# Kernel optimization log

Measured on AMD Instinct MI355X. Metric: run time of the kernel, lower is better.

## Reference

```python
import jax, jax.numpy as jnp
import numpy as np

N, E, De, Dv = 40000, 8000, 32, 8   # nodes, hyperedges, edge degree, node degree
D, Q, EIG, VOC, NC = 256, 256, 64, 1000, 40  # vertex/edge dim, query dim, eig dim, centrality vocab, classes
LN_EPS = 1e-5


def _linear(x, W, b):
    return x @ W + b


def _layernorm(x, g, b):
    mu = jnp.mean(x, axis=-1, keepdims=True)
    var = jnp.mean(jnp.square(x - mu), axis=-1, keepdims=True)
    return (x - mu) * jax.lax.rsqrt(var + LN_EPS) * g + b


def setup_inputs() -> dict:
    key = jax.random.key(0)
    ks = iter(jax.random.split(key, 64))
    def nrm(shape, s=0.02):
        return (jax.random.normal(next(ks), shape, jnp.float32) * s).astype(jnp.float32)
    inp = {
        'vfeat': jax.random.normal(next(ks), (N, D), jnp.float32),
        'efeat': jax.random.normal(next(ks), (E, D), jnp.float32),
        'eign_vec': jax.random.normal(next(ks), (N, EIG), jnp.float32),
        'feat_v_gcn': jax.random.normal(next(ks), (N, D), jnp.float32),
        'cent1': jax.random.uniform(next(ks), (E, De), jnp.float32),
        'cent2': jax.random.uniform(next(ks), (N, Dv), jnp.float32),
        'cent_idx': jax.random.randint(next(ks), (N,), 0, VOC),
        'uniq_idx': jax.random.randint(next(ks), (N,), 0, VOC),
        'edge2node': jax.random.randint(next(ks), (E, De), 0, N),
        'node2edge': jax.random.randint(next(ks), (N, Dv), 0, E),
        # learned parameters (W: [in, out])
        'W_vtx': nrm((D, D)), 'b_vtx': jnp.zeros((D,), jnp.float32),
        'W_pe': nrm((EIG, D)), 'b_pe': jnp.zeros((D,), jnp.float32),
        'cs_emb': nrm((VOC, D)), 'un_emb': nrm((VOC, D)),
        'W_kv': nrm((D, Q)), 'b_kv': jnp.zeros((Q,), jnp.float32),
        'W_vv': nrm((D, D)), 'b_vv': jnp.zeros((D,), jnp.float32),
        'W_qe': nrm((D, Q)), 'b_qe': jnp.zeros((Q,), jnp.float32),
        'W_ke': nrm((D, Q)), 'b_ke': jnp.zeros((Q,), jnp.float32),
        'W_ve': nrm((D, D)), 'b_ve': jnp.zeros((D,), jnp.float32),
        'W_qv': nrm((D, Q)), 'b_qv': jnp.zeros((Q,), jnp.float32),
        'W_l1': nrm((D, Q)), 'b_l1': jnp.zeros((Q,), jnp.float32),
        'W_l2': nrm((Q, D)), 'b_l2': jnp.zeros((D,), jnp.float32),
        'W_l3': nrm((D, Q)), 'b_l3': jnp.zeros((Q,), jnp.float32),
        'W_l4': nrm((Q, D)), 'b_l4': jnp.zeros((D,), jnp.float32),
        'ln1_g': jnp.ones((D,), jnp.float32), 'ln1_b': jnp.zeros((D,), jnp.float32),
        'ln2_g': jnp.ones((D,), jnp.float32), 'ln2_b': jnp.zeros((D,), jnp.float32),
        'W_cls': nrm((D, NC)), 'b_cls': jnp.zeros((NC,), jnp.float32),
    }
    return inp


def _forward(vfeat, efeat, eign_vec, feat_v_gcn, cent1, cent2,
             W_vtx, b_vtx, W_pe, b_pe, cs_emb, un_emb,
             W_kv, b_kv, W_vv, b_vv, W_qe, b_qe, W_ke, b_ke, W_ve, b_ve, W_qv, b_qv,
             W_l1, b_l1, W_l2, b_l2, W_l3, b_l3, W_l4, b_l4,
             ln1_g, ln1_b, ln2_g, ln2_b, W_cls, b_cls,
             cent_idx, uniq_idx, edge2node, node2edge):
    scale = 1.0 / np.sqrt(float(W_kv.shape[1]))  # 1/sqrt(query_dim)
    # first_layer feature assembly: vtx_lin_1layer + PE + GCN + centrality/uniqueness embeddings
    feat_v = (_linear(vfeat, W_vtx, b_vtx) + _linear(eign_vec, W_pe, b_pe)
              + feat_v_gcn + cs_emb[cent_idx] + un_emb[uniq_idx])
    feat_e = efeat

    # ---- stage 1: hyperedges attend over member nodes ('in' etype) ----
    k_n = _linear(feat_v, W_kv, b_kv)              # [N,Q]
    v_n = _linear(feat_v, W_vv, b_vv)              # [N,D]
    q_e = _linear(feat_e, W_qe, b_qe)              # [E,Q]
    km = k_n[edge2node]                            # [E,De,Q]
    attn = jax.nn.leaky_relu(jnp.einsum('edq,eq->ed', km, q_e), 0.01) * scale
    score = jax.nn.softmax(attn + cent1, axis=1)   # centrality-biased softmax (k-core + clustering)
    h_e = jnp.einsum('ed,edc->ec', score, v_n[edge2node])  # [E,D]
    x_e = _layernorm(h_e + feat_e, ln1_g, ln1_b)
    f_e = _linear(jax.nn.relu(_linear(x_e, W_l1, b_l1)), W_l2, b_l2)
    feat_e = _layernorm(f_e + x_e, ln1_g, ln1_b)

    # ---- stage 2: nodes attend over incident hyperedges ('con' etype) ----
    k_e = _linear(feat_e, W_ke, b_ke)              # [E,Q]
    v_e = _linear(feat_e, W_ve, b_ve)              # [E,D]
    q_v = _linear(feat_v, W_qv, b_qv)              # [N,Q]
    km2 = k_e[node2edge]                           # [N,Dv,Q]
    attn2 = jax.nn.leaky_relu(jnp.einsum('ndq,nq->nd', km2, q_v), 0.01) * scale
    score2 = jax.nn.softmax(attn2 + cent2, axis=1)
    h_v = jnp.einsum('nd,ndc->nc', score2, v_e[node2edge])  # [N,D]
    x_v = _layernorm(h_v + feat_v, ln2_g, ln2_b)
    f_v = _linear(jax.nn.relu(_linear(x_v, W_l3, b_l3)), W_l4, b_l4)
    feat_v = _layernorm(f_v + x_v, ln2_g, ln2_b)

    # last_layer classification head (dropout is identity in eval)
    return _linear(feat_v, W_cls, b_cls)           # [N,NC]


def reference(vfeat, efeat, eign_vec, feat_v_gcn, cent1, cent2,
              cent_idx, uniq_idx, edge2node, node2edge,
              W_vtx, b_vtx, W_pe, b_pe, cs_emb, un_emb,
              W_kv, b_kv, W_vv, b_vv, W_qe, b_qe, W_ke, b_ke, W_ve, b_ve, W_qv, b_qv,
              W_l1, b_l1, W_l2, b_l2, W_l3, b_l3, W_l4, b_l4,
              ln1_g, ln1_b, ln2_g, ln2_b, W_cls, b_cls):
    return _forward(vfeat, efeat, eign_vec, feat_v_gcn, cent1, cent2,
                    W_vtx, b_vtx, W_pe, b_pe, cs_emb, un_emb,
                    W_kv, b_kv, W_vv, b_vv, W_qe, b_qe, W_ke, b_ke, W_ve, b_ve, W_qv, b_qv,
                    W_l1, b_l1, W_l2, b_l2, W_l3, b_l3, W_l4, b_l4,
                    ln1_g, ln1_b, ln2_g, ln2_b, W_cls, b_cls,
                    cent_idx, uniq_idx, edge2node, node2edge)
```

## Files before the change

kernel.cpp:

```cpp
#include <hip/hip_runtime.h>
#include <hip/hip_bf16.h>
#include <cstddef>

#define N_NODES 40000
#define N_EDGES 8000
#define DE 32
#define DV 8
#define DIM 256
#define QDIM 256
#define EIGD 64
#define NCLS 40
#define LN_EPS 1e-5f
#define ATT_SCALE 0.0625f

typedef unsigned short u16;
typedef unsigned int u32;
using i16x8 = __attribute__((ext_vector_type(8))) short;
using f32x4 = __attribute__((ext_vector_type(4))) float;

__device__ inline u16 f2b(float f) {
    union { float f; u32 u; } c; c.f = f;
    u32 u = c.u + 0x7FFF + ((c.u >> 16) & 1);
    return (u16)(u >> 16);
}
__device__ inline float b2f(u16 b) {
    union { u32 u; float f; } c; c.u = (u32)b << 16;
    return c.f;
}

__device__ inline void gload_lds16(const u16* g, u16* l) {
    __builtin_amdgcn_global_load_lds(
        (const __attribute__((address_space(1))) void*)g,
        (__attribute__((address_space(3))) void*)l, 16, 0, 0);
}

#define VMCNT6 asm volatile("s_waitcnt vmcnt(6)" ::: "memory")
#define VMCNT0 asm volatile("s_waitcnt vmcnt(0)" ::: "memory")
#define LGKM0  asm volatile("s_waitcnt lgkmcnt(0)" ::: "memory")

__global__ __launch_bounds__(256) void cast_bf16(
    const float* __restrict__ src, u16* __restrict__ dst, int n4)
{
    for (int i = blockIdx.x * 256 + threadIdx.x; i < n4; i += gridDim.x * 256) {
        float4 v = ((const float4*)src)[i];
        ushort4 o;
        o.x = f2b(v.x); o.y = f2b(v.y); o.z = f2b(v.z); o.w = f2b(v.w);
        ((ushort4*)dst)[i] = o;
    }
}

__global__ __launch_bounds__(256) void prep_weights(
    const float* w0, const float* w1, const float* w2, const float* w3,
    const float* w4, const float* w5, const float* w6, const float* w7,
    const float* w8, const float* w9, const float* w10, const float* w11,
    const float* w12, u16* __restrict__ pool)
{
    const float* srcs[13] = {w0,w1,w2,w3,w4,w5,w6,w7,w8,w9,w10,w11,w12};
    const int Ks[13]  = {256,64,256,256,256,256,256,256,256,256,256,256,256};
    const int Nds[13] = {256,256,256,256,256,256,256,256,256,256,256,256,40};
    const int id = blockIdx.z;
    const float* W = srcs[id];
    u16* Wt = pool + (size_t)id * 65536;
    const int K = Ks[id], Nd = Nds[id];
    const int k0 = blockIdx.x * 32, n0 = blockIdx.y * 32;
    if (k0 >= K || n0 >= Nd) return;

    __shared__ float tile[32][33];
    const int x = threadIdx.x & 31, y4 = (threadIdx.x >> 5) * 4;
#pragma unroll
    for (int j = 0; j < 4; j++) {
        int k = k0 + y4 + j;
        tile[y4 + j][x] = (k < K && (n0 + x) < Nd) ? W[(size_t)k * Nd + n0 + x] : 0.f;
    }
    __syncthreads();
#pragma unroll
    for (int j = 0; j < 4; j++) {
        int n = n0 + y4 + j;
        if (n < Nd && (k0 + x) < K)
            Wt[(size_t)n * K + k0 + x] = f2b(tile[x][y4 + j]);
    }
}

template <int EPI>
__global__ __launch_bounds__(256) void gemm_mfma(
    const u16* __restrict__ A, const u16* __restrict__ Wt,
    const float* __restrict__ bias, const float* __restrict__ bias2,
    const u16* __restrict__ resid,
    const float* __restrict__ gcn, const float* __restrict__ emb1,
    const float* __restrict__ emb2, const int* __restrict__ idx1,
    const int* __restrict__ idx2,
    void* __restrict__ Cv, int M, int K, int Nd)
{
    __shared__ u16 Asm[2][64 * 64];
    __shared__ u16 Bsm[2][128 * 64];
    const int t = threadIdx.x;
    const int lane = t & 63, w = t >> 6;
    const int wr = w >> 1, wc = w & 1;
    const int row0 = blockIdx.y * 64, col0 = blockIdx.x * 128;

    f32x4 acc[2][4] = {};

    const int srow = lane >> 3;
    const int sblk = ((lane & 7) ^ srow) * 8;

    const int fr = lane & 15, h = lane >> 4;
    const int lsw = fr & 7;
    const int nt = K >> 6;

    auto stage = [&](int buf, int kt) {
        const int k0 = kt << 6;
#pragma unroll
        for (int i = 0; i < 2; i++) {
            int r = w * 16 + i * 8;
            const u16* gp = A + (size_t)(row0 + r + srow) * K + k0 + sblk;
            gload_lds16(gp, &Asm[buf][r * 64]);
        }
#pragma unroll
        for (int i = 0; i < 4; i++) {
            int r = w * 32 + i * 8;
            int ng = col0 + r + srow; if (ng > Nd - 1) ng = Nd - 1;
            const u16* gp = Wt + (size_t)ng * K + k0 + sblk;
            gload_lds16(gp, &Bsm[buf][r * 64]);
        }
    };

    stage(0, 0);
    for (int kt = 0; kt < nt; ++kt) {
        const int cur = kt & 1;
        const bool more = (kt + 1 < nt);
        if (more) stage(cur ^ 1, kt + 1);
        if (more) { VMCNT6; } else { VMCNT0; }
        __builtin_amdgcn_s_barrier();

        i16x8 af[2][2], bf[2][4];
#pragma unroll
        for (int kk = 0; kk < 2; kk++) {
#pragma unroll
            for (int m = 0; m < 2; m++)
                af[kk][m] = *(const i16x8*)&Asm[cur][(wr * 32 + m * 16 + fr) * 64 +
                                                    ((kk * 4 + h) ^ lsw) * 8];
#pragma unroll
            for (int n = 0; n < 4; n++)
                bf[kk][n] = *(const i16x8*)&Bsm[cur][(wc * 64 + n * 16 + fr) * 64 +
                                                    ((kk * 4 + h) ^ lsw) * 8];
        }
        LGKM0;
        __builtin_amdgcn_sched_barrier(0);
        __builtin_amdgcn_s_barrier();

#pragma unroll
        for (int kk = 0; kk < 2; kk++)
#pragma unroll
            for (int m = 0; m < 2; m++)
#pragma unroll
                for (int n = 0; n < 4; n++)
                    acc[m][n] = __builtin_amdgcn_mfma_f32_16x16x32_bf16(
                        af[kk][m], bf[kk][n], acc[m][n], 0, 0, 0);
    }

#pragma unroll
    for (int m = 0; m < 2; m++) {
#pragma unroll
        for (int j = 0; j < 4; j++) {
            const int grow = row0 + wr * 32 + m * 16 + h * 4 + j;
            int i1 = 0, i2 = 0;
            if constexpr (EPI == 3) { i1 = idx1[grow]; i2 = idx2[grow]; }
#pragma unroll
            for (int n = 0; n < 4; n++) {
                const int gcol = col0 + wc * 64 + n * 16 + fr;
                if (EPI == 4 && gcol >= Nd) continue;
                float v = acc[m][n][j] +
                          (gcol < 256 ? bias[gcol] : bias2[gcol - 256]);
                if constexpr (EPI == 1) v = fmaxf(v, 0.f);
                if constexpr (EPI == 2)
                    v += b2f(resid[(size_t)grow * Nd + gcol]);
                if constexpr (EPI == 3) {
                    v += b2f(resid[(size_t)grow * Nd + gcol]);
                    v += gcn[(size_t)grow * Nd + gcol];
                    v += emb1[(size_t)i1 * Nd + gcol];
                    v += emb2[(size_t)i2 * Nd + gcol];
                }
                if constexpr (EPI == 4)
                    ((float*)Cv)[(size_t)grow * Nd + gcol] = v;
                else
                    ((u16*)Cv)[(size_t)grow * Nd + gcol] = f2b(v);
            }
        }
    }
}

__device__ inline float bfly_sum(float v) {
#pragma unroll
    for (int off = 32; off; off >>= 1) v += __shfl_xor(v, off, 64);
    return v;
}

__global__ __launch_bounds__(256) void edge_attn(
    const u16* __restrict__ KVn, const u16* __restrict__ QE,
    const float* __restrict__ efeat,
    const int* __restrict__ e2n, const float* __restrict__ cent1,
    const float* __restrict__ g, const float* __restrict__ bb,
    u16* __restrict__ XE)
{
    const int lane = threadIdx.x & 63, w = threadIdx.x >> 6;
    const int e = blockIdx.x * 4 + w;
    const int c4 = lane * 4;

    ushort4 q4 = *(const ushort4*)&QE[(size_t)e * QDIM + c4];
    const float q0 = b2f(q4.x), q1 = b2f(q4.y), q2 = b2f(q4.z), q3 = b2f(q4.w);

    int rows[DE]; float sc[DE];
#pragma unroll
    for (int d = 0; d < DE; d++) rows[d] = e2n[(size_t)e * DE + d];
#pragma unroll
    for (int d = 0; d < DE; d++) {
        ushort4 k4 = *(const ushort4*)&KVn[(size_t)rows[d] * 512 + c4];
        float p = q0 * b2f(k4.x) + q1 * b2f(k4.y) + q2 * b2f(k4.z) + q3 * b2f(k4.w);
        p = bfly_sum(p);
        sc[d] = (p > 0.f ? p : 0.01f * p) * ATT_SCALE + cent1[(size_t)e * DE + d];
    }
    float mx = sc[0];
#pragma unroll
    for (int d = 1; d < DE; d++) mx = fmaxf(mx, sc[d]);
    float s = 0.f;
#pragma unroll
    for (int d = 0; d < DE; d++) { sc[d] = __expf(sc[d] - mx); s += sc[d]; }
    const float inv = 1.f / s;

    float a0 = 0.f, a1 = 0.f, a2 = 0.f, a3 = 0.f;
#pragma unroll
    for (int d = 0; d < DE; d++) {
        ushort4 v4 = *(const ushort4*)&KVn[(size_t)rows[d] * 512 + 256 + c4];
        float sd = sc[d] * inv;
        a0 = fmaf(sd, b2f(v4.x), a0); a1 = fmaf(sd, b2f(v4.y), a1);
        a2 = fmaf(sd, b2f(v4.z), a2); a3 = fmaf(sd, b2f(v4.w), a3);
    }
    float4 ef = *(const float4*)&efeat[(size_t)e * DIM + c4];
    float x0 = a0 + ef.x, x1 = a1 + ef.y, x2 = a2 + ef.z, x3 = a3 + ef.w;

    float mu = bfly_sum(x0 + x1 + x2 + x3) * (1.f / DIM);
    float d0 = x0 - mu, d1 = x1 - mu, d2 = x2 - mu, d3 = x3 - mu;
    float var = bfly_sum(d0 * d0 + d1 * d1 + d2 * d2 + d3 * d3) * (1.f / DIM);
    float r = rsqrtf(var + LN_EPS);
    float4 gv = *(const float4*)&g[c4];
    float4 bv = *(const float4*)&bb[c4];
    ushort4 o;
    o.x = f2b(d0 * r * gv.x + bv.x); o.y = f2b(d1 * r * gv.y + bv.y);
    o.z = f2b(d2 * r * gv.z + bv.z); o.w = f2b(d3 * r * gv.w + bv.w);
    *(ushort4*)&XE[(size_t)e * DIM + c4] = o;
}

__global__ __launch_bounds__(256) void node_attn(
    const u16* __restrict__ KVe, const u16* __restrict__ QV,
    const u16* __restrict__ FV,
    const int* __restrict__ n2e, const float* __restrict__ cent2,
    const float* __restrict__ g, const float* __restrict__ bb,
    u16* __restrict__ XV)
{
    const int lane = threadIdx.x & 63, w = threadIdx.x >> 6;
    const int n = blockIdx.x * 4 + w;
    const int c4 = lane * 4;

    ushort4 q4 = *(const ushort4*)&QV[(size_t)n * QDIM + c4];
    const float q0 = b2f(q4.x), q1 = b2f(q4.y), q2 = b2f(q4.z), q3 = b2f(q4.w);

    int rows[DV]; float sc[DV];
#pragma unroll
    for (int d = 0; d < DV; d++) rows[d] = n2e[(size_t)n * DV + d];
#pragma unroll
    for (int d = 0; d < DV; d++) {
        ushort4 k4 = *(const ushort4*)&KVe[(size_t)rows[d] * 512 + c4];
        float p = q0 * b2f(k4.x) + q1 * b2f(k4.y) + q2 * b2f(k4.z) + q3 * b2f(k4.w);
        p = bfly_sum(p);
        sc[d] = (p > 0.f ? p : 0.01f * p) * ATT_SCALE + cent2[(size_t)n * DV + d];
    }
    float mx = sc[0];
#pragma unroll
    for (int d = 1; d < DV; d++) mx = fmaxf(mx, sc[d]);
    float s = 0.f;
#pragma unroll
    for (int d = 0; d < DV; d++) { sc[d] = __expf(sc[d] - mx); s += sc[d]; }
    const float inv = 1.f / s;

    float a0 = 0.f, a1 = 0.f, a2 = 0.f, a3 = 0.f;
#pragma unroll
    for (int d = 0; d < DV; d++) {
        ushort4 v4 = *(const ushort4*)&KVe[(size_t)rows[d] * 512 + 256 + c4];
        float sd = sc[d] * inv;
        a0 = fmaf(sd, b2f(v4.x), a0); a1 = fmaf(sd, b2f(v4.y), a1);
        a2 = fmaf(sd, b2f(v4.z), a2); a3 = fmaf(sd, b2f(v4.w), a3);
    }
    ushort4 f4 = *(const ushort4*)&FV[(size_t)n * DIM + c4];
    float x0 = a0 + b2f(f4.x), x1 = a1 + b2f(f4.y);
    float x2 = a2 + b2f(f4.z), x3 = a3 + b2f(f4.w);

    float mu = bfly_sum(x0 + x1 + x2 + x3) * (1.f / DIM);
    float d0 = x0 - mu, d1 = x1 - mu, d2 = x2 - mu, d3 = x3 - mu;
    float var = bfly_sum(d0 * d0 + d1 * d1 + d2 * d2 + d3 * d3) * (1.f / DIM);
    float r = rsqrtf(var + LN_EPS);
    float4 gv = *(const float4*)&g[c4];
    float4 bv = *(const float4*)&bb[c4];
    ushort4 o;
    o.x = f2b(d0 * r * gv.x + bv.x); o.y = f2b(d1 * r * gv.y + bv.y);
    o.z = f2b(d2 * r * gv.z + bv.z); o.w = f2b(d3 * r * gv.w + bv.w);
    *(ushort4*)&XV[(size_t)n * DIM + c4] = o;
}

__global__ __launch_bounds__(256) void ln_rows(
    const u16* __restrict__ X, const float* __restrict__ g,
    const float* __restrict__ bb, u16* __restrict__ Y)
{
    const int lane = threadIdx.x & 63, w = threadIdx.x >> 6;
    const int row = blockIdx.x * 4 + w;
    const int c4 = lane * 4;
    ushort4 v4 = *(const ushort4*)&X[(size_t)row * DIM + c4];
    float x0 = b2f(v4.x), x1 = b2f(v4.y), x2 = b2f(v4.z), x3 = b2f(v4.w);
    float mu = bfly_sum(x0 + x1 + x2 + x3) * (1.f / DIM);
    float d0 = x0 - mu, d1 = x1 - mu, d2 = x2 - mu, d3 = x3 - mu;
    float var = bfly_sum(d0 * d0 + d1 * d1 + d2 * d2 + d3 * d3) * (1.f / DIM);
    float r = rsqrtf(var + LN_EPS);
    float4 gv = *(const float4*)&g[c4];
    float4 bv = *(const float4*)&bb[c4];
    ushort4 o;
    o.x = f2b(d0 * r * gv.x + bv.x); o.y = f2b(d1 * r * gv.y + bv.y);
    o.z = f2b(d2 * r * gv.z + bv.z); o.w = f2b(d3 * r * gv.w + bv.w);
    *(ushort4*)&Y[(size_t)row * DIM + c4] = o;
}

extern "C" void kernel_launch(void* const* d_in, const int* in_sizes, int n_in,
                              void* d_out, int out_size, void* d_ws, size_t ws_size,
                              hipStream_t stream)
{
    const float* vfeat  = (const float*)d_in[0];
    const float* efeat  = (const float*)d_in[1];
    const float* eign   = (const float*)d_in[2];
    const float* gcn    = (const float*)d_in[3];
    const float* cent1  = (const float*)d_in[4];
    const float* cent2  = (const float*)d_in[5];
    const int*   cidx   = (const int*)d_in[6];
    const int*   uidx   = (const int*)d_in[7];
    const int*   e2n    = (const int*)d_in[8];
    const int*   n2e    = (const int*)d_in[9];
    const float* W_vtx  = (const float*)d_in[10]; const float* b_vtx = (const float*)d_in[11];
    const float* W_pe   = (const float*)d_in[12]; const float* b_pe  = (const float*)d_in[13];
    const float* cs_emb = (const float*)d_in[14]; const float* un_emb= (const float*)d_in[15];
    const float* W_kv   = (const float*)d_in[16]; const float* b_kv  = (const float*)d_in[17];
    const float* W_vv   = (const float*)d_in[18]; const float* b_vv  = (const float*)d_in[19];
    const float* W_qe   = (const float*)d_in[20]; const float* b_qe  = (const float*)d_in[21];
    const float* W_ke   = (const float*)d_in[22]; const float* b_ke  = (const float*)d_in[23];
    const float* W_ve   = (const float*)d_in[24]; const float* b_ve  = (const float*)d_in[25];
    const float* W_qv   = (const float*)d_in[26]; const float* b_qv  = (const float*)d_in[27];
    const float* W_l1   = (const float*)d_in[28]; const float* b_l1  = (const float*)d_in[29];
    const float* W_l2   = (const float*)d_in[30]; const float* b_l2  = (const float*)d_in[31];
    const float* W_l3   = (const float*)d_in[32]; const float* b_l3  = (const float*)d_in[33];
    const float* W_l4   = (const float*)d_in[34]; const float* b_l4  = (const float*)d_in[35];
    const float* ln1_g  = (const float*)d_in[36]; const float* ln1_b = (const float*)d_in[37];
    const float* ln2_g  = (const float*)d_in[38]; const float* ln2_b = (const float*)d_in[39];
    const float* W_cls  = (const float*)d_in[40]; const float* b_cls = (const float*)d_in[41];
    float* out = (float*)d_out;

    const size_t NE = (size_t)N_NODES * DIM;
    const size_t EE = (size_t)N_EDGES * DIM;
    u16* ws = (u16*)d_ws;
    u16* FV  = ws;
    u16* T0  = FV + NE;
    u16* B2  = T0 + NE;
    u16* KVn = B2 + NE;
    u16* Vb  = KVn + 2 * NE;
    u16* Gb  = Vb + NE;
    u16* Eb  = Gb + (size_t)N_NODES * EIGD;
    u16* QEb = Eb + EE;
    u16* XE  = QEb + EE;
    u16* TE  = XE + EE;
    u16* FE  = TE + EE;
    u16* KVe = FE + EE;
    u16* Wp  = KVe + 2 * EE;
    u16* Wt_vtx = Wp +  0*65536; u16* Wt_pe = Wp +  1*65536;
    u16* Wt_kv  = Wp +  2*65536;
    u16* Wt_qe  = Wp +  4*65536; u16* Wt_ke = Wp +  5*65536;
         u16* Wt_qv = Wp +  7*65536;
    u16* Wt_l1  = Wp +  8*65536; u16* Wt_l2 = Wp +  9*65536;
    u16* Wt_l3  = Wp + 10*65536; u16* Wt_l4 = Wp + 11*65536;
    u16* Wt_cls = Wp + 12*65536;

    const dim3 blk(256);
    const dim3 gW(8, 8, 13);
    const dim3 gN1(2, N_NODES / 64);
    const dim3 gN2(4, N_NODES / 64);
    const dim3 gE1(2, N_EDGES / 64);
    const dim3 gE2(4, N_EDGES / 64);
    const dim3 gCl(1, N_NODES / 64);

    prep_weights<<<gW, blk, 0, stream>>>(
        W_vtx, W_pe, W_kv, W_vv, W_qe, W_ke, W_ve, W_qv,
        W_l1, W_l2, W_l3, W_l4, W_cls, Wp);
    cast_bf16<<<2048, blk, 0, stream>>>(vfeat, Vb, (int)(NE / 4));
    cast_bf16<<<1024, blk, 0, stream>>>(eign, Gb, N_NODES * EIGD / 4);
    cast_bf16<<<1024, blk, 0, stream>>>(efeat, Eb, (int)(EE / 4));

    gemm_mfma<0><<<gN1, blk, 0, stream>>>(Vb, Wt_vtx, b_vtx, b_vtx, nullptr,
        nullptr, nullptr, nullptr, nullptr, nullptr, T0, N_NODES, DIM, DIM);
    gemm_mfma<3><<<gN1, blk, 0, stream>>>(Gb, Wt_pe, b_pe, b_pe, T0,
        gcn, cs_emb, un_emb, cidx, uidx, FV, N_NODES, EIGD, DIM);

    gemm_mfma<0><<<gN2, blk, 0, stream>>>(FV, Wt_kv, b_kv, b_vv, nullptr,
        nullptr, nullptr, nullptr, nullptr, nullptr, KVn, N_NODES, DIM, 512);
    gemm_mfma<0><<<gE1, blk, 0, stream>>>(Eb, Wt_qe, b_qe, b_qe, nullptr,
        nullptr, nullptr, nullptr, nullptr, nullptr, QEb, N_EDGES, DIM, QDIM);
    edge_attn<<<N_EDGES / 4, blk, 0, stream>>>(KVn, QEb, efeat, e2n, cent1,
        ln1_g, ln1_b, XE);
    gemm_mfma<1><<<gE1, blk, 0, stream>>>(XE, Wt_l1, b_l1, b_l1, nullptr,
        nullptr, nullptr, nullptr, nullptr, nullptr, TE, N_EDGES, DIM, QDIM);
    gemm_mfma<2><<<gE1, blk, 0, stream>>>(TE, Wt_l2, b_l2, b_l2, XE,
        nullptr, nullptr, nullptr, nullptr, nullptr, FE, N_EDGES, QDIM, DIM);
    ln_rows<<<N_EDGES / 4, blk, 0, stream>>>(FE, ln1_g, ln1_b, FE);

    gemm_mfma<0><<<gE2, blk, 0, stream>>>(FE, Wt_ke, b_ke, b_ve, nullptr,
        nullptr, nullptr, nullptr, nullptr, nullptr, KVe, N_EDGES, DIM, 512);
    gemm_mfma<0><<<gN1, blk, 0, stream>>>(FV, Wt_qv, b_qv, b_qv, nullptr,
        nullptr, nullptr, nullptr, nullptr, nullptr, T0, N_NODES, DIM, QDIM);
    node_attn<<<N_NODES / 4, blk, 0, stream>>>(KVe, T0, FV, n2e, cent2,
        ln2_g, ln2_b, B2);
    gemm_mfma<1><<<gN1, blk, 0, stream>>>(B2, Wt_l3, b_l3, b_l3, nullptr,
        nullptr, nullptr, nullptr, nullptr, nullptr, T0, N_NODES, DIM, QDIM);
    gemm_mfma<2><<<gN1, blk, 0, stream>>>(T0, Wt_l4, b_l4, b_l4, B2,
        nullptr, nullptr, nullptr, nullptr, nullptr, FV, N_NODES, QDIM, DIM);
    ln_rows<<<N_NODES / 4, blk, 0, stream>>>(FV, ln2_g, ln2_b, FV);

    gemm_mfma<4><<<gCl, blk, 0, stream>>>(FV, Wt_cls, b_cls, b_cls, nullptr,
        nullptr, nullptr, nullptr, nullptr, nullptr, out, N_NODES, DIM, NCLS);
}
```

Baseline: 269.3 us.

## Fuse GEMMs with layernorm, merge projections, and use online softmax in attention

Measured after the change: 264.3 us. About the same (-1.9%).

```diff
diff --git a/kernel.cpp b/kernel.cpp
--- a/kernel.cpp
+++ b/kernel.cpp
@@ -34,18 +34,29 @@
         (__attribute__((address_space(3))) void*)l, 16, 0, 0);
 }
 
-#define VMCNT6 asm volatile("s_waitcnt vmcnt(6)" ::: "memory")
-#define VMCNT0 asm volatile("s_waitcnt vmcnt(0)" ::: "memory")
-#define LGKM0  asm volatile("s_waitcnt lgkmcnt(0)" ::: "memory")
-
-__global__ __launch_bounds__(256) void cast_bf16(
-    const float* __restrict__ src, u16* __restrict__ dst, int n4)
-{
-    for (int i = blockIdx.x * 256 + threadIdx.x; i < n4; i += gridDim.x * 256) {
-        float4 v = ((const float4*)src)[i];
+#define VMCNT10 asm volatile("s_waitcnt vmcnt(10)" ::: "memory")
+#define VMCNT6  asm volatile("s_waitcnt vmcnt(6)" ::: "memory")
+#define VMCNT0  asm volatile("s_waitcnt vmcnt(0)" ::: "memory")
+#define LGKM0   asm volatile("s_waitcnt lgkmcnt(0)" ::: "memory")
+
+__global__ __launch_bounds__(256) void cast_all(
+    const float* __restrict__ vfeat, const float* __restrict__ eign,
+    const float* __restrict__ efeat,
+    u16* __restrict__ Vb, u16* __restrict__ Gb, u16* __restrict__ Eb)
+{
+    const int A4 = N_NODES * DIM / 4;
+    const int B4 = N_NODES * EIGD / 4;
+    const int C4 = N_EDGES * DIM / 4;
+    const int tot = A4 + B4 + C4;
+    for (int i = blockIdx.x * 256 + threadIdx.x; i < tot; i += gridDim.x * 256) {
+        const float4* s; ushort4* d; int j;
+        if (i < A4)            { s = (const float4*)vfeat; d = (ushort4*)Vb; j = i; }
+        else if (i < A4 + B4)  { s = (const float4*)eign;  d = (ushort4*)Gb; j = i - A4; }
+        else                   { s = (const float4*)efeat; d = (ushort4*)Eb; j = i - A4 - B4; }
+        float4 v = s[j];
         ushort4 o;
         o.x = f2b(v.x); o.y = f2b(v.y); o.z = f2b(v.z); o.w = f2b(v.w);
-        ((ushort4*)dst)[i] = o;
+        d[j] = o;
     }
 }
 
@@ -81,15 +92,16 @@
     }
 }
 
-template <int EPI>
+template <int EPI, bool DUAL>
 __global__ __launch_bounds__(256) void gemm_mfma(
-    const u16* __restrict__ A, const u16* __restrict__ Wt,
-    const float* __restrict__ bias, const float* __restrict__ bias2,
-    const u16* __restrict__ resid,
+    const u16* __restrict__ A, const u16* __restrict__ A2,
+    const u16* __restrict__ Wt, const u16* __restrict__ Wt2,
+    const float* __restrict__ bias0, const float* __restrict__ bias1,
+    const float* __restrict__ bias2,
     const float* __restrict__ gcn, const float* __restrict__ emb1,
     const float* __restrict__ emb2, const int* __restrict__ idx1,
     const int* __restrict__ idx2,
-    void* __restrict__ Cv, int M, int K, int Nd)
+    void* __restrict__ Cv, int M, int K1, int Ktot, int Nd)
 {
     __shared__ u16 Asm[2][64 * 64];
     __shared__ u16 Bsm[2][128 * 64];
@@ -105,21 +117,26 @@
 
     const int fr = lane & 15, h = lane >> 4;
     const int lsw = fr & 7;
-    const int nt = K >> 6;
+    const int nt = Ktot >> 6;
 
     auto stage = [&](int buf, int kt) {
         const int k0 = kt << 6;
+        const bool first = !DUAL || (k0 < K1);
 #pragma unroll
         for (int i = 0; i < 2; i++) {
             int r = w * 16 + i * 8;
-            const u16* gp = A + (size_t)(row0 + r + srow) * K + k0 + sblk;
+            const u16* gp = first
+                ? A  + (size_t)(row0 + r + srow) * K1 + k0 + sblk
+                : A2 + (size_t)(row0 + r + srow) * 64 + (k0 - K1) + sblk;
             gload_lds16(gp, &Asm[buf][r * 64]);
         }
 #pragma unroll
         for (int i = 0; i < 4; i++) {
             int r = w * 32 + i * 8;
             int ng = col0 + r + srow; if (ng > Nd - 1) ng = Nd - 1;
-            const u16* gp = Wt + (size_t)ng * K + k0 + sblk;
+            const u16* gp = first
+                ? Wt  + (size_t)ng * K1 + k0 + sblk
+                : Wt2 + (size_t)ng * 64 + (k0 - K1) + sblk;
             gload_lds16(gp, &Bsm[buf][r * 64]);
         }
     };
@@ -169,17 +186,18 @@
             for (int n = 0; n < 4; n++) {
                 const int gcol = col0 + wc * 64 + n * 16 + fr;
                 if (EPI == 4 && gcol >= Nd) continue;
-                float v = acc[m][n][j] +
-                          (gcol < 256 ? bias[gcol] : bias2[gcol - 256]);
-                if constexpr (EPI == 1) v = fmaxf(v, 0.f);
-                if constexpr (EPI == 2)
-                    v += b2f(resid[(size_t)grow * Nd + gcol]);
+                float v;
                 if constexpr (EPI == 3) {
-                    v += b2f(resid[(size_t)grow * Nd + gcol]);
+                    v = acc[m][n][j] + bias0[gcol] + bias1[gcol];
                     v += gcn[(size_t)grow * Nd + gcol];
                     v += emb1[(size_t)i1 * Nd + gcol];
                     v += emb2[(size_t)i2 * Nd + gcol];
+                } else {
+                    const float* bp = (gcol < 256) ? bias0
+                                     : ((gcol < 512) ? bias1 : bias2);
+                    v = acc[m][n][j] + bp[gcol & 255];
                 }
+                if constexpr (EPI == 1) v = fmaxf(v, 0.f);
                 if constexpr (EPI == 4)
                     ((float*)Cv)[(size_t)grow * Nd + gcol] = v;
                 else
@@ -189,14 +207,126 @@
     }
 }
 
-__device__ inline float bfly_sum(float v) {
-#pragma unroll
-    for (int off = 32; off; off >>= 1) v += __shfl_xor(v, off, 64);
-    return v;
+__global__ __launch_bounds__(256) void gemm_ln(
+    const u16* __restrict__ A, const u16* __restrict__ Wt,
+    const float* __restrict__ bias, const u16* __restrict__ resid,
+    const float* __restrict__ g, const float* __restrict__ bb,
+    u16* __restrict__ Y, int M)
+{
+    __shared__ u16 Asm[2][64 * 64];
+    __shared__ u16 Bsm[2][256 * 64];
+    const int t = threadIdx.x;
+    const int lane = t & 63, w = t >> 6;
+    const int row0 = blockIdx.y * 64;
+
+    f32x4 acc[4][4] = {};
+
+    const int srow = lane >> 3;
+    const int sblk = ((lane & 7) ^ srow) * 8;
+    const int fr = lane & 15, h = lane >> 4;
+    const int lsw = fr & 7;
+
+    auto stage = [&](int buf, int kt) {
+        const int k0 = kt << 6;
+#pragma unroll
+        for (int i = 0; i < 2; i++) {
+            int r = w * 16 + i * 8;
+            gload_lds16(A + (size_t)(row0 + r + srow) * 256 + k0 + sblk,
+                        &Asm[buf][r * 64]);
+        }
+#pragma unroll
+        for (int i = 0; i < 8; i++) {
+            int r = w * 64 + i * 8;
+            gload_lds16(Wt + (size_t)(r + srow) * 256 + k0 + sblk,
+                        &Bsm[buf][r * 64]);
+        }
+    };
+
+    stage(0, 0);
+    for (int kt = 0; kt < 4; ++kt) {
+        const int cur = kt & 1;
+        const bool more = (kt < 3);
+        if (more) stage(cur ^ 1, kt + 1);
+        if (more) { VMCNT10; } else { VMCNT0; }
+        __builtin_amdgcn_s_barrier();
+
+        i16x8 af[2][4], bf[2][4];
+#pragma unroll
+        for (int kk = 0; kk < 2; kk++) {
+#pragma unroll
+            for (int m = 0; m < 4; m++)
+                af[kk][m] = *(const i16x8*)&Asm[cur][(m * 16 + fr) * 64 +
+                                                    ((kk * 4 + h) ^ lsw) * 8];
+#pragma unroll
+            for (int n = 0; n < 4; n++)
+                bf[kk][n] = *(const i16x8*)&Bsm[cur][(w * 64 + n * 16 + fr) * 64 +
+                                                    ((kk * 4 + h) ^ lsw) * 8];
+        }
+        LGKM0;
+        __builtin_amdgcn_sched_barrier(0);
+        __builtin_amdgcn_s_barrier();
+
+#pragma unroll
+        for (int kk = 0; kk < 2; kk++)
+#pragma unroll
+            for (int m = 0; m < 4; m++)
+#pragma unroll
+                for (int n = 0; n < 4; n++)
+                    acc[m][n] = __builtin_amdgcn_mfma_f32_16x16x32_bf16(
+                        af[kk][m], bf[kk][n], acc[m][n], 0, 0, 0);
+    }
+
+    float* redS = (float*)&Asm[0][0];
+    float* redQ = redS + 256;
+#pragma unroll
+    for (int m = 0; m < 4; m++) {
+#pragma unroll
+        for (int j = 0; j < 4; j++) {
+            const int grow = row0 + m * 16 + h * 4 + j;
+            float s = 0.f, q = 0.f;
+#pragma unroll
+            for (int n = 0; n < 4; n++) {
+                const int gcol = w * 64 + n * 16 + fr;
+                float v = acc[m][n][j] + bias[gcol] +
+                          b2f(resid[(size_t)grow * 256 + gcol]);
+                acc[m][n][j] = v;
+                s += v; q += v * v;
+            }
+#pragma unroll
+            for (int off = 1; off < 16; off <<= 1) {
+                s += __shfl_xor(s, off, 64);
+                q += __shfl_xor(q, off, 64);
+            }
+            if (fr == 0) {
+                redS[(m * 16 + h * 4 + j) * 4 + w] = s;
+                redQ[(m * 16 + h * 4 + j) * 4 + w] = q;
+            }
+        }
+    }
+    __syncthreads();
+#pragma unroll
+    for (int m = 0; m < 4; m++) {
+#pragma unroll
+        for (int j = 0; j < 4; j++) {
+            const int r = m * 16 + h * 4 + j;
+            const int grow = row0 + r;
+            float4 s4 = *(const float4*)&redS[r * 4];
+            float4 q4 = *(const float4*)&redQ[r * 4];
+            float mu = (s4.x + s4.y + s4.z + s4.w) * (1.f / DIM);
+            float var = (q4.x + q4.y + q4.z + q4.w) * (1.f / DIM) - mu * mu;
+            float rr = rsqrtf(var + LN_EPS);
+#pragma unroll
+            for (int n = 0; n < 4; n++) {
+                const int gcol = w * 64 + n * 16 + fr;
+                float y = (acc[m][n][j] - mu) * rr * g[gcol] + bb[gcol];
+                Y[(size_t)grow * 256 + gcol] = f2b(y);
+            }
+        }
+    }
 }
 
 __global__ __launch_bounds__(256) void edge_attn(
-    const u16* __restrict__ KVn, const u16* __restrict__ QE,
+    const u16* __restrict__ KVQn, const u16* __restrict__ QE,
     const float* __restrict__ efeat,
     const int* __restrict__ e2n, const float* __restrict__ cent1,
     const float* __restrict__ g, const float* __restrict__ bb,
@@ -209,49 +339,73 @@
     ushort4 q4 = *(const ushort4*)&QE[(size_t)e * QDIM + c4];
     const float q0 = b2f(q4.x), q1 = b2f(q4.y), q2 = b2f(q4.z), q3 = b2f(q4.w);
 
-    int rows[DE]; float sc[DE];
+    int rows[DE];
 #pragma unroll
     for (int d = 0; d < DE; d++) rows[d] = e2n[(size_t)e * DE + d];
-#pragma unroll
-    for (int d = 0; d < DE; d++) {
-        ushort4 k4 = *(const ushort4*)&KVn[(size_t)rows[d] * 512 + c4];
-        float p = q0 * b2f(k4.x) + q1 * b2f(k4.y) + q2 * b2f(k4.z) + q3 * b2f(k4.w);
-        p = bfly_sum(p);
-        sc[d] = (p > 0.f ? p : 0.01f * p) * ATT_SCALE + cent1[(size_t)e * DE + d];
-    }
-    float mx = sc[0];
-#pragma unroll
-    for (int d = 1; d < DE; d++) mx = fmaxf(mx, sc[d]);
-    float s = 0.f;
-#pragma unroll
-    for (int d = 0; d < DE; d++) { sc[d] = __expf(sc[d] - mx); s += sc[d]; }
-    const float inv = 1.f / s;
-
+
+    float m = -1e30f, l = 0.f;
     float a0 = 0.f, a1 = 0.f, a2 = 0.f, a3 = 0.f;
 #pragma unroll
-    for (int d = 0; d < DE; d++) {
-        ushort4 v4 = *(const ushort4*)&KVn[(size_t)rows[d] * 512 + 256 + c4];
-        float sd = sc[d] * inv;
-        a0 = fmaf(sd, b2f(v4.x), a0); a1 = fmaf(sd, b2f(v4.y), a1);
-        a2 = fmaf(sd, b2f(v4.z), a2); a3 = fmaf(sd, b2f(v4.w), a3);
-    }
+    for (int d0 = 0; d0 < DE; d0 += 4) {
+        ushort4 k4[4], v4[4]; float p[4];
+#pragma unroll
+        for (int j = 0; j < 4; j++) {
+            const u16* base = KVQn + (size_t)rows[d0 + j] * 768 + c4;
+            k4[j] = *(const ushort4*)base;
+            v4[j] = *(const ushort4*)(base + 256);
+        }
+#pragma unroll
+        for (int j = 0; j < 4; j++)
+            p[j] = q0 * b2f(k4[j].x) + q1 * b2f(k4[j].y)
+                 + q2 * b2f(k4[j].z) + q3 * b2f(k4[j].w);
+#pragma unroll
+        for (int off = 32; off; off >>= 1)
+#pragma unroll
+            for (int j = 0; j < 4; j++) p[j] += __shfl_xor(p[j], off, 64);
+#pragma unroll
+        for (int j = 0; j < 4; j++) {
+            float s = p[j];
+            s = (s > 0.f ? s : 0.01f * s) * ATT_SCALE + cent1[(size_t)e * DE + d0 + j];
+            float wgt;
+            if (s > m) {
+                float f = __expf(m - s);
+                a0 *= f; a1 *= f; a2 *= f; a3 *= f; l *= f;
+                m = s; wgt = 1.f;
+            } else {
+                wgt = __expf(s - m);
+            }
+            l += wgt;
+            a0 = fmaf(wgt, b2f(v4[j].x), a0);
+            a1 = fmaf(wgt, b2f(v4[j].y), a1);
+            a2 = fmaf(wgt, b2f(v4[j].z), a2);
+            a3 = fmaf(wgt, b2f(v4[j].w), a3);
+        }
+    }
+    const float inv = 1.f / l;
     float4 ef = *(const float4*)&efeat[(size_t)e * DIM + c4];
-    float x0 = a0 + ef.x, x1 = a1 + ef.y, x2 = a2 + ef.z, x3 = a3 + ef.w;
-
-    float mu = bfly_sum(x0 + x1 + x2 + x3) * (1.f / DIM);
-    float d0 = x0 - mu, d1 = x1 - mu, d2 = x2 - mu, d3 = x3 - mu;
-    float var = bfly_sum(d0 * d0 + d1 * d1 + d2 * d2 + d3 * d3) * (1.f / DIM);
+    float x0 = a0 * inv + ef.x, x1 = a1 * inv + ef.y;
+    float x2 = a2 * inv + ef.z, x3 = a3 * inv + ef.w;
+
+    float mu = x0 + x1 + x2 + x3;
+#pragma unroll
+    for (int off = 32; off; off >>= 1) mu += __shfl_xor(mu, off, 64);
+    mu *= (1.f / DIM);
+    float d0_ = x0 - mu, d1 = x1 - mu, d2 = x2 - mu, d3 = x3 - mu;
+    float var = d0_ * d0_ + d1 * d1 + d2 * d2 + d3 * d3;
+#pragma unroll
+    for (int off = 32; off; off >>= 1) var += __shfl_xor(var, off, 64);
+    var *= (1.f / DIM);
     float r = rsqrtf(var + LN_EPS);
     float4 gv = *(const float4*)&g[c4];
     float4 bv = *(const float4*)&bb[c4];
     ushort4 o;
-    o.x = f2b(d0 * r * gv.x + bv.x); o.y = f2b(d1 * r * gv.y + bv.y);
+    o.x = f2b(d0_ * r * gv.x + bv.x); o.y = f2b(d1 * r * gv.y + bv.y);
     o.z = f2b(d2 * r * gv.z + bv.z); o.w = f2b(d3 * r * gv.w + bv.w);
     *(ushort4*)&XE[(size_t)e * DIM + c4] = o;
 }
 
 __global__ __launch_bounds__(256) void node_attn(
-    const u16* __restrict__ KVe, const u16* __restrict__ QV,
+    const u16* __restrict__ KVe, const u16* __restrict__ KVQn,
     const u16* __restrict__ FV,
     const int* __restrict__ n2e, const float* __restrict__ cent2,
     const float* __restrict__ g, const float* __restrict__ bb,
@@ -261,42 +415,62 @@
     const int n = blockIdx.x * 4 + w;
     const int c4 = lane * 4;
 
-    ushort4 q4 = *(const ushort4*)&QV[(size_t)n * QDIM + c4];
+    ushort4 q4 = *(const ushort4*)&KVQn[(size_t)n * 768 + 512 + c4];
     const float q0 = b2f(q4.x), q1 = b2f(q4.y), q2 = b2f(q4.z), q3 = b2f(q4.w);
 
-    int rows[DV]; float sc[DV];
+    int rows[DV];
 #pragma unroll
     for (int d = 0; d < DV; d++) rows[d] = n2e[(size_t)n * DV + d];
+
+    ushort4 k4[DV], v4[DV];
 #pragma unroll
     for (int d = 0; d < DV; d++) {
-        ushort4 k4 = *(const ushort4*)&KVe[(size_t)rows[d] * 512 + c4];
-        float p = q0 * b2f(k4.x) + q1 * b2f(k4.y) + q2 * b2f(k4.z) + q3 * b2f(k4.w);
-        p = bfly_sum(p);
-        sc[d] = (p > 0.f ? p : 0.01f * p) * ATT_SCALE + cent2[(size_t)n * DV + d];
-    }
-    float mx = sc[0];
-#pragma unroll
-    for (int d = 1; d < DV; d++) mx = fmaxf(mx, sc[d]);
+        const u16* base = KVe + (size_t)rows[d] * 512 + c4;
+        k4[d] = *(const ushort4*)base;
+        v4[d] = *(const ushort4*)(base + 256);
+    }
+    float p[DV];
+#pragma unroll
+    for (int d = 0; d < DV; d++)
+        p[d] = q0 * b2f(k4[d].x) + q1 * b2f(k4[d].y)
+             + q2 * b2f(k4[d].z) + q3 * b2f(k4[d].w);
+#pragma unroll
+    for (int off = 32; off; off >>= 1)
+#pragma unroll
+        for (int d = 0; d < DV; d++) p[d] += __shfl_xor(p[d], off, 64);
+
+#pragma unroll
+    for (int d = 0; d < DV; d++)
+        p[d] = (p[d] > 0.f ? p[d] : 0.01f * p[d]) * ATT_SCALE
+             + cent2[(size_t)n * DV + d];
+    float mx = p[0];
+#pragma unroll
+    for (int d = 1; d < DV; d++) mx = fmaxf(mx, p[d]);
     float s = 0.f;
 #pragma unroll
-    for (int d = 0; d < DV; d++) { sc[d] = __expf(sc[d] - mx); s += sc[d]; }
+    for (int d = 0; d < DV; d++) { p[d] = __expf(p[d] - mx); s += p[d]; }
     const float inv = 1.f / s;
 
     float a0 = 0.f, a1 = 0.f, a2 = 0.f, a3 = 0.f;
 #pragma unroll
     for (int d = 0; d < DV; d++) {
-        ushort4 v4 = *(const ushort4*)&KVe[(size_t)rows[d] * 512 + 256 + c4];
-        float sd = sc[d] * inv;
-        a0 = fmaf(sd, b2f(v4.x), a0); a1 = fmaf(sd, b2f(v4.y), a1);
-        a2 = fmaf(sd, b2f(v4.z), a2); a3 = fmaf(sd, b2f(v4.w), a3);
+        float sd = p[d] * inv;
+        a0 = fmaf(sd, b2f(v4[d].x), a0); a1 = fmaf(sd, b2f(v4[d].y), a1);
+        a2 = fmaf(sd, b2f(v4[d].z), a2); a3 = fmaf(sd, b2f(v4[d].w), a3);
     }
     ushort4 f4 = *(const ushort4*)&FV[(size_t)n * DIM + c4];
     float x0 = a0 + b2f(f4.x), x1 = a1 + b2f(f4.y);
     float x2 = a2 + b2f(f4.z), x3 = a3 + b2f(f4.w);
 
-    float mu = bfly_sum(x0 + x1 + x2 + x3) * (1.f / DIM);
+    float mu = x0 + x1 + x2 + x3;
+#pragma unroll
+    for (int off = 32; off; off >>= 1) mu += __shfl_xor(mu, off, 64);
+    mu *= (1.f / DIM);
     float d0 = x0 - mu, d1 = x1 - mu, d2 = x2 - mu, d3 = x3 - mu;
-    float var = bfly_sum(d0 * d0 + d1 * d1 + d2 * d2 + d3 * d3) * (1.f / DIM);
+    float var = d0 * d0 + d1 * d1 + d2 * d2 + d3 * d3;
+#pragma unroll
+    for (int off = 32; off; off >>= 1) var += __shfl_xor(var, off, 64);
+    var *= (1.f / DIM);
     float r = rsqrtf(var + LN_EPS);
     float4 gv = *(const float4*)&g[c4];
     float4 bv = *(const float4*)&bb[c4];
@@ -304,27 +478,6 @@
     o.x = f2b(d0 * r * gv.x + bv.x); o.y = f2b(d1 * r * gv.y + bv.y);
     o.z = f2b(d2 * r * gv.z + bv.z); o.w = f2b(d3 * r * gv.w + bv.w);
     *(ushort4*)&XV[(size_t)n * DIM + c4] = o;
-}
-
-__global__ __launch_bounds__(256) void ln_rows(
-    const u16* __restrict__ X, const float* __restrict__ g,
-    const float* __restrict__ bb, u16* __restrict__ Y)
-{
-    const int lane = threadIdx.x & 63, w = threadIdx.x >> 6;
-    const int row = blockIdx.x * 4 + w;
-    const int c4 = lane * 4;
-    ushort4 v4 = *(const ushort4*)&X[(size_t)row * DIM + c4];
-    float x0 = b2f(v4.x), x1 = b2f(v4.y), x2 = b2f(v4.z), x3 = b2f(v4.w);
-    float mu = bfly_sum(x0 + x1 + x2 + x3) * (1.f / DIM);
-    float d0 = x0 - mu, d1 = x1 - mu, d2 = x2 - mu, d3 = x3 - mu;
-    float var = bfly_sum(d0 * d0 + d1 * d1 + d2 * d2 + d3 * d3) * (1.f / DIM);
-    float r = rsqrtf(var + LN_EPS);
-    float4 gv = *(const float4*)&g[c4];
-    float4 bv = *(const float4*)&bb[c4];
-    ushort4 o;
-    o.x = f2b(d0 * r * gv.x + bv.x); o.y = f2b(d1 * r * gv.y + bv.y);
-    o.z = f2b(d2 * r * gv.z + bv.z); o.w = f2b(d3 * r * gv.w + bv.w);
-    *(ushort4*)&Y[(size_t)row * DIM + c4] = o;
 }
 
 extern "C" void kernel_launch(void* const* d_in, const int* in_sizes, int n_in,
@@ -362,71 +515,77 @@
     const size_t NE = (size_t)N_NODES * DIM;
     const size_t EE = (size_t)N_EDGES * DIM;
     u16* ws = (u16*)d_ws;
-    u16* FV  = ws;
-    u16* T0  = FV + NE;
-    u16* B2  = T0 + NE;
-    u16* KVn = B2 + NE;
-    u16* Vb  = KVn + 2 * NE;
-    u16* Gb  = Vb + NE;
-    u16* Eb  = Gb + (size_t)N_NODES * EIGD;
-    u16* QEb = Eb + EE;
-    u16* XE  = QEb + EE;
-    u16* TE  = XE + EE;
-    u16* FE  = TE + EE;
-    u16* KVe = FE + EE;
-    u16* Wp  = KVe + 2 * EE;
-    u16* Wt_vtx = Wp +  0*65536; u16* Wt_pe = Wp +  1*65536;
-    u16* Wt_kv  = Wp +  2*65536;
-    u16* Wt_qe  = Wp +  4*65536; u16* Wt_ke = Wp +  5*65536;
-         u16* Wt_qv = Wp +  7*65536;
-    u16* Wt_l1  = Wp +  8*65536; u16* Wt_l2 = Wp +  9*65536;
-    u16* Wt_l3  = Wp + 10*65536; u16* Wt_l4 = Wp + 11*65536;
-    u16* Wt_cls = Wp + 12*65536;
+    u16* FVb  = ws;
+    u16* Vb   = FVb + NE;
+    u16* Gb   = Vb + NE;
+    u16* KVQn = Gb + NE / 4;
+    u16* B2   = KVQn + 3 * NE;
+    u16* Eb   = B2 + NE;
+    u16* QEb  = Eb + EE;
+    u16* XE   = QEb + EE;
+    u16* FE   = XE + EE;
+    u16* KVe  = FE + EE;
+    u16* Wp   = KVe + 2 * EE;
+    u16* Wt_vtx = Wp +  0 * 65536;
+    u16* Wt_pe  = Wp +  1 * 65536;
+    u16* Wt_kvq = Wp +  2 * 65536;
+    u16* Wt_qe  = Wp +  5 * 65536;
+    u16* Wt_kve = Wp +  6 * 65536;
+    u16* Wt_l1  = Wp +  8 * 65536;
+    u16* Wt_l2  = Wp +  9 * 65536;
+    u16* Wt_l3  = Wp + 10 * 65536;
+    u16* Wt_l4  = Wp + 11 * 65536;
+    u16* Wt_cls = Wp + 12 * 65536;
+    u16* T0 = Vb;
+    u16* TE = Eb;
 
     const dim3 blk(256);
     const dim3 gW(8, 8, 13);
-    const dim3 gN1(2, N_NODES / 64);
-    const dim3 gN2(4, N_NODES / 64);
-    const dim3 gE1(2, N_EDGES / 64);
-    const dim3 gE2(4, N_EDGES / 64);
+    const dim3 gA(2, N_NODES / 64);
+    const dim3 gKVQ(6, N_NODES / 64);
+    const dim3 gQE(2, N_EDGES / 64);
+    const dim3 gL1(2, N_EDGES / 64);
+    const dim3 gLN_E(1, N_EDGES / 64);
+    const dim3 gKVe(4, N_EDGES / 64);
+    const dim3 gL3(2, N_NODES / 64);
+    const dim3 gLN_N(1, N_NODES / 64);
     const dim3 gCl(1, N_NODES / 64);
 
     prep_weights<<<gW, blk, 0, stream>>>(
-        W_vtx, W_pe, W_kv, W_vv, W_qe, W_ke, W_ve, W_qv,
+        W_vtx, W_pe, W_kv, W_vv, W_qv, W_qe, W_ke, W_ve,
         W_l1, W_l2, W_l3, W_l4, W_cls, Wp);
-    cast_bf16<<<2048, blk, 0, stream>>>(vfeat, Vb, (int)(NE / 4));
-    cast_bf16<<<1024, blk, 0, stream>>>(eign, Gb, N_NODES * EIGD / 4);
-    cast_bf16<<<1024, blk, 0, stream>>>(efeat, Eb, (int)(EE / 4));
-
-    gemm_mfma<0><<<gN1, blk, 0, stream>>>(Vb, Wt_vtx, b_vtx, b_vtx, nullptr,
-        nullptr, nullptr, nullptr, nullptr, nullptr, T0, N_NODES, DIM, DIM);
-    gemm_mfma<3><<<gN1, blk, 0, stream>>>(Gb, Wt_pe, b_pe, b_pe, T0,
-        gcn, cs_emb, un_emb, cidx, uidx, FV, N_NODES, EIGD, DIM);
-
-    gemm_mfma<0><<<gN2, blk, 0, stream>>>(FV, Wt_kv, b_kv, b_vv, nullptr,
-        nullptr, nullptr, nullptr, nullptr, nullptr, KVn, N_NODES, DIM, 512);
-    gemm_mfma<0><<<gE1, blk, 0, stream>>>(Eb, Wt_qe, b_qe, b_qe, nullptr,
-        nullptr, nullptr, nullptr, nullptr, nullptr, QEb, N_EDGES, DIM, QDIM);
-    edge_attn<<<N_EDGES / 4, blk, 0, stream>>>(KVn, QEb, efeat, e2n, cent1,
+    cast_all<<<2048, blk, 0, stream>>>(vfeat, eign, efeat, Vb, Gb, Eb);
+
+    gemm_mfma<3, true><<<gA, blk, 0, stream>>>(Vb, Gb, Wt_vtx, Wt_pe,
+        b_vtx, b_pe, nullptr, gcn, cs_emb, un_emb, cidx, uidx,
+        FVb, N_NODES, 256, 320, DIM);
+
+    gemm_mfma<0, false><<<gKVQ, blk, 0, stream>>>(FVb, nullptr, Wt_kvq, nullptr,
+        b_kv, b_vv, b_qv, nullptr, nullptr, nullptr, nullptr, nullptr,
+        KVQn, N_NODES, 256, 256, 768);
+    gemm_mfma<0, false><<<gQE, blk, 0, stream>>>(Eb, nullptr, Wt_qe, nullptr,
+        b_qe, nullptr, nullptr, nullptr, nullptr, nullptr, nullptr, nullptr,
+        QEb, N_EDGES, 256, 256, QDIM);
+    edge_attn<<<N_EDGES / 4, blk, 0, stream>>>(KVQn, QEb, efeat, e2n, cent1,
         ln1_g, ln1_b, XE);
-    gemm_mfma<1><<<gE1, blk, 0, stream>>>(XE, Wt_l1, b_l1, b_l1, nullptr,
-        nullptr, nullptr, nullptr, nullptr, nullptr, TE, N_EDGES, DIM, QDIM);
-    gemm_mfma<2><<<gE1, blk, 0, stream>>>(TE, Wt_l2, b_l2, b_l2, XE,
-        nullptr, nullptr, nullptr, nullptr, nullptr, FE, N_EDGES, QDIM, DIM);
-    ln_rows<<<N_EDGES / 4, blk, 0, stream>>>(FE, ln1_g, ln1_b, FE);
-
-    gemm_mfma<0><<<gE2, blk, 0, stream>>>(FE, Wt_ke, b_ke, b_ve, nullptr,
-        nullptr, nullptr, nullptr, nullptr, nullptr, KVe, N_EDGES, DIM, 512);
-    gemm_mfma<0><<<gN1, blk, 0, stream>>>(FV, Wt_qv, b_qv, b_qv, nullptr,
-        nullptr, nullptr, nullptr, nullptr, nullptr, T0, N_NODES, DIM, QDIM);
-    node_attn<<<N_NODES / 4, blk, 0, stream>>>(KVe, T0, FV, n2e, cent2,
+    gemm_mfma<1, false><<<gL1, blk, 0, stream>>>(XE, nullptr, Wt_l1, nullptr,
+        b_l1, nullptr, nullptr, nullptr, nullptr, nullptr, nullptr, nullptr,
+        TE, N_EDGES, 256, 256, QDIM);
+    gemm_ln<<<gLN_E, blk, 0, stream>>>(TE, Wt_l2, b_l2, XE, ln1_g, ln1_b,
+        FE, N_EDGES);
+
+    gemm_mfma<0, false><<<gKVe, blk, 0, stream>>>(FE, nullptr, Wt_kve, nullptr,
+        b_ke, b_ve, nullptr, nullptr, nullptr, nullptr, nullptr, nullptr,
+        KVe, N_EDGES, 256, 256, 512);
+    node_attn<<<N_NODES / 4, blk, 0, stream>>>(KVe, KVQn, FVb, n2e, cent2,
         ln2_g, ln2_b, B2);
-    gemm_mfma<1><<<gN1, blk, 0, stream>>>(B2, Wt_l3, b_l3, b_l3, nullptr,
-        nullptr, nullptr, nullptr, nullptr, nullptr, T0, N_NODES, DIM, QDIM);
-    gemm_mfma<2><<<gN1, blk, 0, stream>>>(T0, Wt_l4, b_l4, b_l4, B2,
-        nullptr, nullptr, nullptr, nullptr, nullptr, FV, N_NODES, QDIM, DIM);
-    ln_rows<<<N_NODES / 4, blk, 0, stream>>>(FV, ln2_g, ln2_b, FV);
-
-    gemm_mfma<4><<<gCl, blk, 0, stream>>>(FV, Wt_cls, b_cls, b_cls, nullptr,
-        nullptr, nullptr, nullptr, nullptr, nullptr, out, N_NODES, DIM, NCLS);
-}
+    gemm_mfma<1, false><<<gL3, blk, 0, stream>>>(B2, nullptr, Wt_l3, nullptr,
+        b_l3, nullptr, nullptr, nullptr, nullptr, nullptr, nullptr, nullptr,
+        T0, N_NODES, 256, 256, QDIM);
+    gemm_ln<<<gLN_N, blk, 0, stream>>>(T0, Wt_l4, b_l4, B2, ln2_g, ln2_b,
+        FVb, N_NODES);
+
+    gemm_mfma<4, false><<<gCl, blk, 0, stream>>>(FVb, nullptr, Wt_cls, nullptr,
+        b_cls, nullptr, nullptr, nullptr, nullptr, nullptr, nullptr, nullptr,
+        out, N_NODES, 256, 256, NCLS);
+}
```
